# Performance work log

Hardware: AMD Instinct MI355X
Metric: run time of the kernel (lower is better)

Reference implementation:

```python
import jax, jax.numpy as jnp
import numpy as np


def setup_inputs() -> dict:
    key = jax.random.key(0)
    k1, k2 = jax.random.split(key)
    B, N, D = 8, 256, 128
    x = jax.random.normal(k1, (B, N, D), dtype=jnp.float32)
    # Dense edge layer: maps 2D -> D (concat of the two node embeddings).
    W = jax.random.normal(k2, (2 * D, D), dtype=jnp.float32) * (1.0 / np.sqrt(2 * D))
    b = jnp.zeros((D,), dtype=jnp.float32)
    return {"x": x, "W": W, "b": b}


def reference(x, W, b):
    # PairwiseEdgeEmbeddings: e[b,i,j] = concat(x[b,i], x[b,j])  -> (B,N,N,2D)
    # Edge layer: relu(e @ W + b)                                 -> (B,N,N,D)
    # Faithful but efficient: concat @ W == x_i @ W1 + x_j @ W2 with W=[W1;W2],
    # avoiding materializing the (B,N,N,2D) concat tensor.
    D = x.shape[-1]
    W1, W2 = W[:D], W[D:]
    a = jnp.einsum('bnd,df->bnf', x, W1)  # contribution of node i
    c = jnp.einsum('bnd,df->bnf', x, W2)  # contribution of node j
    edges = jax.nn.relu(a[:, :, None, :] + c[:, None, :, :] + b)  # (B,N,N,D)
    # Reduce layer: sum over j -> node embeddings (B,N,D)
    return edges.sum(axis=2)
```

## Files before the change

kernel.cpp:

```cpp
#include <hip/hip_runtime.h>

typedef float f32x4 __attribute__((ext_vector_type(4)));

#define B_ 8
#define N_ 256
#define D_ 128

__global__ __launch_bounds__(512) void onepass_relational_kernel(
    const float* __restrict__ x, const float* __restrict__ W,
    const float* __restrict__ bias, float* __restrict__ out) {

    __shared__ f32x4 Wc[256];
    __shared__ f32x4 AS[256];
    __shared__ f32x4 CS[256];
    __shared__ f32x4 PR[256];

    const int tid = threadIdx.x;
    const int bid = blockIdx.x;
    const int b   = bid & 7;
    const int f0  = (bid >> 3) * 4;

    if (tid < 256) {
        Wc[tid] = *reinterpret_cast<const f32x4*>(W + (size_t)tid * D_ + f0);
    }
    __syncthreads();

    const int r    = tid & 255;
    const int half = tid >> 8;
    const float* __restrict__ xr = x + ((size_t)b * N_ + r) * D_;
    const f32x4* __restrict__ Wh = &Wc[half * 128];

    f32x4 acc = {0.f, 0.f, 0.f, 0.f};
    #pragma unroll 8
    for (int d4 = 0; d4 < 32; ++d4) {
        const f32x4 xv = *reinterpret_cast<const f32x4*>(xr + d4 * 4);
        acc += xv[0] * Wh[d4 * 4 + 0] + xv[1] * Wh[d4 * 4 + 1] +
               xv[2] * Wh[d4 * 4 + 2] + xv[3] * Wh[d4 * 4 + 3];
    }

    if (half) {
        CS[r] = acc;
    } else {
        AS[r] = acc + *reinterpret_cast<const f32x4*>(bias + f0);
    }
    __syncthreads();

    const f32x4 zero = {0.f, 0.f, 0.f, 0.f};
    const f32x4 av = AS[r];
    const f32x4* __restrict__ Cj = &CS[half * 128];
    f32x4 s = zero;
    #pragma unroll 8
    for (int j = 0; j < 128; ++j) {
        s += __builtin_elementwise_max(av + Cj[j], zero);
    }

    if (half) PR[r] = s;
    __syncthreads();
    if (!half) {
        s += PR[r];
        *reinterpret_cast<f32x4*>(out + ((size_t)b * N_ + r) * D_ + f0) = s;
    }
}

extern "C" void kernel_launch(void* const* d_in, const int* in_sizes, int n_in,
                              void* d_out, int out_size, void* d_ws, size_t ws_size,
                              hipStream_t stream) {
    const float* x    = (const float*)d_in[0];
    const float* W    = (const float*)d_in[1];
    const float* bias = (const float*)d_in[2];
    float* out = (float*)d_out;

    onepass_relational_kernel<<<B_ * (D_ / 4), 512, 0, stream>>>(x, W, bias, out);
}
```

Baseline: 19.27 us.

## Register-block rows and split reductions across threads in projection and pair-sum

Each thread now handles four rows instead of one. In the projection, the D dimension is split four ways and the partial sums are combined through shared memory. In the pairwise relu-sum, the j range is split into eight groups, and a tree reduction with extra barriers combines them. The aim is to reuse each W and C value loaded from shared memory across four rows, cutting LDS traffic per FMA. The cost is more registers, a larger shared-memory partial buffer, and several additional __syncthreads.

```diff
diff --git a/kernel.cpp b/kernel.cpp
--- a/kernel.cpp
+++ b/kernel.cpp
@@ -6,14 +6,14 @@
 #define N_ 256
 #define D_ 128
 
-__global__ __launch_bounds__(512) void onepass_relational_kernel(
+__global__ __launch_bounds__(512) void onepass_rb_kernel(
     const float* __restrict__ x, const float* __restrict__ W,
     const float* __restrict__ bias, float* __restrict__ out) {
 
     __shared__ f32x4 Wc[256];
     __shared__ f32x4 AS[256];
     __shared__ f32x4 CS[256];
-    __shared__ f32x4 PR[256];
+    __shared__ f32x4 PR[1536];
 
     const int tid = threadIdx.x;
     const int bid = blockIdx.x;
@@ -25,40 +25,93 @@
     }
     __syncthreads();
 
-    const int r    = tid & 255;
-    const int half = tid >> 8;
-    const float* __restrict__ xr = x + ((size_t)b * N_ + r) * D_;
-    const f32x4* __restrict__ Wh = &Wc[half * 128];
+    const int rq = tid & 63;
+    const int hq = (tid >> 6) & 1;
+    const int dq = tid >> 7;
 
-    f32x4 acc = {0.f, 0.f, 0.f, 0.f};
-    #pragma unroll 8
-    for (int d4 = 0; d4 < 32; ++d4) {
-        const f32x4 xv = *reinterpret_cast<const f32x4*>(xr + d4 * 4);
-        acc += xv[0] * Wh[d4 * 4 + 0] + xv[1] * Wh[d4 * 4 + 1] +
-               xv[2] * Wh[d4 * 4 + 2] + xv[3] * Wh[d4 * 4 + 3];
+    f32x4 acc[4] = {};
+    {
+        const float* __restrict__ xbase =
+            x + ((size_t)b * N_ + rq * 4) * D_ + dq * 32;
+        const f32x4* __restrict__ Wh = &Wc[hq * 128 + dq * 32];
+        #pragma unroll
+        for (int c = 0; c < 8; ++c) {
+            f32x4 xv[4];
+            #pragma unroll
+            for (int k = 0; k < 4; ++k)
+                xv[k] = *reinterpret_cast<const f32x4*>(
+                    xbase + (size_t)k * D_ + c * 4);
+            #pragma unroll
+            for (int dd = 0; dd < 4; ++dd) {
+                const f32x4 wv = Wh[c * 4 + dd];
+                #pragma unroll
+                for (int k = 0; k < 4; ++k)
+                    acc[k] += xv[k][dd] * wv;
+            }
+        }
     }
 
-    if (half) {
-        CS[r] = acc;
-    } else {
-        AS[r] = acc + *reinterpret_cast<const f32x4*>(bias + f0);
+    if (dq > 0) {
+        #pragma unroll
+        for (int k = 0; k < 4; ++k)
+            PR[((dq - 1) * 128 + hq * 64 + rq) * 4 + k] = acc[k];
+    }
+    __syncthreads();
+    if (dq == 0) {
+        #pragma unroll
+        for (int s = 0; s < 3; ++s)
+            #pragma unroll
+            for (int k = 0; k < 4; ++k)
+                acc[k] += PR[(s * 128 + hq * 64 + rq) * 4 + k];
+        if (hq == 0) {
+            const f32x4 bv = *reinterpret_cast<const f32x4*>(bias + f0);
+            #pragma unroll
+            for (int k = 0; k < 4; ++k) AS[rq * 4 + k] = acc[k] + bv;
+        } else {
+            #pragma unroll
+            for (int k = 0; k < 4; ++k) CS[rq * 4 + k] = acc[k];
+        }
     }
     __syncthreads();
 
+    const int rg = tid & 63;
+    const int jg = tid >> 6;
     const f32x4 zero = {0.f, 0.f, 0.f, 0.f};
-    const f32x4 av = AS[r];
-    const f32x4* __restrict__ Cj = &CS[half * 128];
-    f32x4 s = zero;
+
+    f32x4 av[4], s2[4];
+    #pragma unroll
+    for (int k = 0; k < 4; ++k) { av[k] = AS[rg * 4 + k]; s2[k] = zero; }
+
+    const f32x4* __restrict__ Cj = &CS[jg * 32];
     #pragma unroll 8
-    for (int j = 0; j < 128; ++j) {
-        s += __builtin_elementwise_max(av + Cj[j], zero);
+    for (int j = 0; j < 32; ++j) {
+        const f32x4 cv = Cj[j];
+        #pragma unroll
+        for (int k = 0; k < 4; ++k)
+            s2[k] += __builtin_elementwise_max(av[k] + cv, zero);
     }
 
-    if (half) PR[r] = s;
-    __syncthreads();
-    if (!half) {
-        s += PR[r];
-        *reinterpret_cast<f32x4*>(out + ((size_t)b * N_ + r) * D_ + f0) = s;
+    #pragma unroll
+    for (int s = 4; s >= 1; s >>= 1) {
+        if (jg >= s && jg < 2 * s) {
+            #pragma unroll
+            for (int k = 0; k < 4; ++k)
+                PR[((jg - s) * 64 + rg) * 4 + k] = s2[k];
+        }
+        __syncthreads();
+        if (jg < s) {
+            #pragma unroll
+            for (int k = 0; k < 4; ++k)
+                s2[k] += PR[(jg * 64 + rg) * 4 + k];
+        }
+        __syncthreads();
+    }
+
+    if (jg == 0) {
+        #pragma unroll
+        for (int k = 0; k < 4; ++k)
+            *reinterpret_cast<f32x4*>(
+                out + ((size_t)b * N_ + rg * 4 + k) * D_ + f0) = s2[k];
     }
 }
 
@@ -70,5 +123,5 @@
     const float* bias = (const float*)d_in[2];
     float* out = (float*)d_out;
 
-    onepass_relational_kernel<<<B_ * (D_ / 4), 512, 0, stream>>>(x, W, bias, out);
+    onepass_rb_kernel<<<B_ * (D_ / 4), 512, 0, stream>>>(x, W, bias, out);
 }
```

Measured after the change: 25.88 us. 1.34x slower.
